# Optimization experiments

Hardware: AMD Instinct MI355X
Metric: run time of the kernel (lower is better)

## Reference

```python
import jax, jax.numpy as jnp
import numpy as np

N = 20000   # nodes
D = 512     # input_dim
H = 256     # hidden_dim = input_dim // 2
C = 7       # class_num
L = 2       # layer_num
E = 131072  # edges per class
B = 8192    # edge pairs to classify
EPS = 1e-5  # BatchNorm eps


def _bn(x, gamma, beta):
    # BatchNorm1d in training mode: batch mean / biased variance
    mu = jnp.mean(x, axis=0)
    var = jnp.mean((x - mu) ** 2, axis=0)
    return (x - mu) * jax.lax.rsqrt(var + EPS) * gamma + beta


def _gcn_conv(x, src, dst, W, b):
    # PyG GCNConv: add self-loops, symmetric deg^-1/2 normalization, aggregate at dst
    n = x.shape[0]
    loop = jnp.arange(n)
    s = jnp.concatenate([src, loop])
    d = jnp.concatenate([dst, loop])
    deg = jax.ops.segment_sum(jnp.ones(s.shape[0], x.dtype), d, num_segments=n)
    dinv = jax.lax.rsqrt(jnp.maximum(deg, 1.0))  # deg >= 1 due to self-loops
    norm = dinv[s] * dinv[d]                     # [E+N]
    xw = x @ W                                   # [N, H]
    out = jax.ops.segment_sum(norm[:, None] * xw[s], d, num_segments=n)
    return out + b


def _comp_gcn(x, edge_index, gW, gb, dW, db):
    row, col = edge_index[0], edge_index[1]
    h = jax.nn.relu(_gcn_conv(x, row, col, gW, gb))
    comp = (x[col] * x[row]) @ dW + db           # diff_proj(x[col]*x[row])
    msg = jax.ops.segment_sum(comp, row, num_segments=x.shape[0])
    return h + msg


def setup_inputs() -> dict:
    key = jax.random.key(0)
    ks = jax.random.split(key, 20)
    s = 0.05
    nrm = lambda k, shape: jax.random.normal(k, shape, jnp.float32) * s
    return {
        "x": jax.random.normal(ks[0], (N, D), jnp.float32),
        "edges": jax.random.randint(ks[1], (C, 2, E), 0, N),
        "node_id": jax.random.randint(ks[2], (2, B), 0, N),
        "lin0_W": nrm(ks[3], (C, D, H)),
        "lin0_b": nrm(ks[4], (C, H)),
        "bn_gamma": jnp.ones((C, H), jnp.float32),
        "bn_beta": jnp.zeros((C, H), jnp.float32),
        "gcn_W": nrm(ks[5], (C, L, H, H)),
        "gcn_b": nrm(ks[6], (C, L, H)),
        "dp_W": nrm(ks[7], (C, L, H, H)),
        "dp_b": nrm(ks[8], (C, L, H)),
        "fc1_W": nrm(ks[9], (C, 3 * H, 3 * H // 2)),
        "fc1_b": nrm(ks[10], (C, 3 * H // 2)),
        "fc2_W": nrm(ks[11], (C, 3 * H // 2, 3 * H // 4)),
        "fc2_b": nrm(ks[12], (C, 3 * H // 4)),
        "fc3_W": nrm(ks[13], (C, 3 * H // 4, H // 16)),
        "fc3_b": nrm(ks[14], (C, H // 16)),
        "cls_W": nrm(ks[15], ((H // 16) * C, C)),
        "cls_b": nrm(ks[16], (C,)),
    }


def reference(x, edges, node_id, lin0_W, lin0_b, bn_gamma, bn_beta,
              gcn_W, gcn_b, dp_W, dp_b, fc1_W, fc1_b, fc2_W, fc2_b,
              fc3_W, fc3_b, cls_W, cls_b):
    src, dst = node_id[0], node_id[1]
    outs = []
    for i in range(C):  # fixed small branch count
        t = jax.nn.relu(_bn(x @ lin0_W[i] + lin0_b[i], bn_gamma[i], bn_beta[i]))
        for j in range(L):
            t = _comp_gcn(t, edges[i], gcn_W[i, j], gcn_b[i, j], dp_W[i, j], dp_b[i, j])
        x1, x2 = t[src], t[dst]                        # [B, H]
        p = jnp.concatenate([x1, x2, x1 * x2], axis=1)  # [B, 3H]
        p = jax.nn.relu(p @ fc1_W[i] + fc1_b[i])
        p = jax.nn.relu(p @ fc2_W[i] + fc2_b[i])
        p = p @ fc3_W[i] + fc3_b[i]                     # [B, H//16]
        outs.append(p)
    r = jax.nn.relu(jnp.concatenate(outs, axis=1))      # [B, C*H//16]
    return r @ cls_W + cls_b                            # [B, C]
```

## Files before the change

### kernel.cpp

```cpp
#include <hip/hip_runtime.h>

typedef unsigned short u16;
typedef unsigned int   u32;
typedef __attribute__((ext_vector_type(8))) short short8;
typedef __attribute__((ext_vector_type(4))) float f32x4;

#define NNODES 20000
#define MPAD   20096
#define DIN    512
#define HID    256
#define NCLS   7
#define NLAY   2
#define NEDGE  131072
#define NPAIR  8192
#define BN_EPS 1e-5f

__device__ __forceinline__ void atomAddF(float* p, float v) { unsafeAtomicAdd(p, v); }

__device__ __forceinline__ float b2f(u16 u) {
    u32 x = ((u32)u) << 16;
    return __builtin_bit_cast(float, x);
}
__device__ __forceinline__ u16 f2b(float f) {
    u32 u = __builtin_bit_cast(u32, f);
    u32 r = u + 0x7FFFu + ((u >> 16) & 1u);
    return (u16)(r >> 16);
}
__device__ __forceinline__ float4 b2f4(ushort4 u) {
    return make_float4(b2f(u.x), b2f(u.y), b2f(u.z), b2f(u.w));
}
__device__ __forceinline__ ushort4 f2b4(float a, float b, float c, float d) {
    ushort4 o; o.x = f2b(a); o.y = f2b(b); o.z = f2b(c); o.w = f2b(d); return o;
}

__device__ __forceinline__ void async_copy16(const u16* g, u16* l) {
    __builtin_amdgcn_global_load_lds((const __attribute__((address_space(1))) void*)g,
                                     (__attribute__((address_space(3))) void*)l, 16, 0, 0);
}

__device__ __forceinline__ int chunk_swz(int orig, int nwg) {
    int xcd = orig & 7, q = nwg >> 3, r = nwg & 7;
    int base = (xcd < r) ? xcd * (q + 1) : r * (q + 1) + (xcd - r) * q;
    return base + (orig >> 3);
}

__global__ __launch_bounds__(256, 2) void gemm_fn(
    const u16* __restrict__ A, size_t sA, const u16* __restrict__ Bt, size_t sB,
    const float* __restrict__ bias, int sBias,
    float* __restrict__ Cf, u16* __restrict__ Cb, size_t sC,
    int M, int N, int K, int relu, float* statsOut)
{
    const int z = blockIdx.z;
    A  += (size_t)z * sA;
    Bt += (size_t)z * sB;
    if (bias) bias += (size_t)z * sBias;

    __shared__ u16 sm[12288];
    __shared__ float sred[512];
    u16* As = sm;
    u16* Bs = sm + 4096;

    const int tid  = threadIdx.x;
    const int wave = tid >> 6;
    const int lane = tid & 63;
    const int bm = blockIdx.x * 128;
    const int wr = (wave >> 1) * 64;
// ... 75 lines not shown
        atomAddF(&statsOut[(size_t)z * 512 + tid], sred[tid]);
        atomAddF(&statsOut[(size_t)z * 512 + 256 + tid], sred[256 + tid]);
    }

    if (Cb && N == 256) {
        u16* R = sm;
        const int lrb = (wave >> 1) * 16 + fq * 4;
        const int cb0 = wc + fr;
        #pragma unroll
        for (int mi = 0; mi < 4; ++mi) {
            __syncthreads();
            #pragma unroll
            for (int ni = 0; ni < 8; ++ni)
                #pragma unroll
                for (int rr = 0; rr < 4; ++rr) {
                    float v = acc[mi][ni][rr] + bv[ni];
                    if (relu) v = fmaxf(v, 0.f);
                    R[(lrb + rr) * 264 + cb0 + ni * 16] = f2b(v);
                }
            __syncthreads();
            #pragma unroll
            for (int p = 0; p < 4; ++p) {
                int idx = p * 256 + tid;
                int lr = idx >> 5, ch = idx & 31;
                int grow = bm + (lr >> 4) * 64 + mi * 16 + (lr & 15);
                if (grow < M)
                    *(short8*)&Cb[(size_t)z * sC + (size_t)grow * 256 + ch * 8] =
                        *(const short8*)&R[lr * 264 + ch * 8];
            }
        }
    } else {
        #pragma unroll
        for (int ni = 0; ni < 8; ++ni) {
            int col = wc + ni * 16 + fr;
            if (col >= N) continue;
            #pragma unroll
            for (int mi = 0; mi < 4; ++mi) {
                int rbase = bm + wr + mi * 16 + fq * 4;
                #pragma unroll
                for (int rr = 0; rr < 4; ++rr) {
                    int row = rbase + rr;
                    if (row >= M) continue;
                    float v = acc[mi][ni][rr] + bv[ni];
                    if (relu) v = fmaxf(v, 0.f);
                    size_t o = (size_t)z * sC + (size_t)row * N + col;
                    if (Cf) Cf[o] = v;
                    if (Cb) Cb[o] = f2b(v);
                }
            }
        }
    }
}

__global__ __launch_bounds__(256, 2) void gemm_dual(
    const u16* U, const u16* __restrict__ V, size_t sAct,
    const u16* __restrict__ Gt, const u16* __restrict__ Dt, size_t sW,
    const float* __restrict__ gbias, const float* __restrict__ dbias, int sBias,
    const float* __restrict__ degf, size_t sDeg,
    u16* Cb, int M)
{
    const int z = blockIdx.z;
    U += (size_t)z * sAct; V += (size_t)z * sAct;
    Gt += (size_t)z * sW;  Dt += (size_t)z * sW;
    gbias += (size_t)z * sBias; dbias += (size_t)z * sBias;
    degf  += (size_t)z * sDeg;
    u16* C = Cb + (size_t)z * sAct;

    __shared__ u16 sm[12288];
    u16* As = sm;
    u16* Bs = sm + 4096;

    const int tid  = threadIdx.x;
    const int wave = tid >> 6;
    const int lane = tid & 63;
    const int bm = blockIdx.x * 128;
    const int wr = (wave >> 1) * 64;
    const int wc = (wave & 1) * 128;

    const int ar = tid >> 2, aj = (tid & 3) * 8;
    u16* AsA = As + tid * 8;
    u16* AsB = As + tid * 8 + 2048;

    const int fr = lane & 15;
    const int fq = lane >> 4;
    const int kg = fq * 8;

    f32x4 zero = {0.f, 0.f, 0.f, 0.f};
    f32x4 acc[4][8];
    #pragma unroll
    for (int mi = 0; mi < 4; ++mi)
        #pragma unroll
        for (int ni = 0; ni < 8; ++ni) acc[mi][ni] = zero;

    for (int k0 = 0; k0 < HID; k0 += 32) {
        async_copy16(U + (size_t)(bm + ar) * HID + aj + k0, AsA);
        async_copy16(U + (size_t)(bm + ar + 64) * HID + aj + k0, AsB);
        #pragma unroll
        for (int c = 0; c < 4; ++c)
            async_copy16(Gt + (size_t)(c * 64 + ar) * HID + aj + k0,
                         Bs + ((size_t)c * 256 + tid) * 8);
        __syncthreads();
        short8 af[4], bfr[8];
        #pragma unroll
        for (int mi = 0; mi < 4; ++mi)
            af[mi] = *(const short8*)&As[(wr + mi * 16 + fr) * 32 + kg];
        #pragma unroll
        for (int ni = 0; ni < 8; ++ni)
            bfr[ni] = *(const short8*)&Bs[(wc + ni * 16 + fr) * 32 + kg];
        #pragma unroll
        for (int mi = 0; mi < 4; ++mi)
            #pragma unroll
            for (int ni = 0; ni < 8; ++ni)
                acc[mi][ni] = __builtin_amdgcn_mfma_f32_16x16x32_bf16(
                    af[mi], bfr[ni], acc[mi][ni], 0, 0, 0);
        __syncthreads();
    }

    {
        float gv[8];
        #pragma unroll
        for (int ni = 0; ni < 8; ++ni) gv[ni] = gbias[wc + ni * 16 + fr];
        #pragma unroll
        for (int mi = 0; mi < 4; ++mi)
            #pragma unroll
            for (int ni = 0; ni < 8; ++ni)
                #pragma unroll
                for (int rr = 0; rr < 4; ++rr)
                    acc[mi][ni][rr] = fmaxf(acc[mi][ni][rr] + gv[ni], 0.f);
    }

    for (int k0 = 0; k0 < HID; k0 += 32) {
        async_copy16(V + (size_t)(bm + ar) * HID + aj + k0, AsA);
        async_copy16(V + (size_t)(bm + ar + 64) * HID + aj + k0, AsB);
        #pragma unroll
        for (int c = 0; c < 4; ++c)
            async_copy16(Dt + (size_t)(c * 64 + ar) * HID + aj + k0,
                         Bs + ((size_t)c * 256 + tid) * 8);
        __syncthreads();
        short8 af[4], bfr[8];
        #pragma unroll
        for (int mi = 0; mi < 4; ++mi)
            af[mi] = *(const short8*)&As[(wr + mi * 16 + fr) * 32 + kg];
        #pragma unroll
        for (int ni = 0; ni < 8; ++ni)
            bfr[ni] = *(const short8*)&Bs[(wc + ni * 16 + fr) * 32 + kg];
        #pragma unroll
        for (int mi = 0; mi < 4; ++mi)
            #pragma unroll
            for (int ni = 0; ni < 8; ++ni)
                acc[mi][ni] = __builtin_amdgcn_mfma_f32_16x16x32_bf16(
                    af[mi], bfr[ni], acc[mi][ni], 0, 0, 0);
        __syncthreads();
    }

    float dv8[8];
    #pragma unroll
    for (int ni = 0; ni < 8; ++ni) dv8[ni] = dbias[wc + ni * 16 + fr];
    u16* R = sm;
    const int lrb = (wave >> 1) * 16 + fq * 4;
    const int cb0 = wc + fr;
    #pragma unroll
    for (int mi = 0; mi < 4; ++mi) {
        __syncthreads();
        float dgr[4];
        #pragma unroll
        for (int rr = 0; rr < 4; ++rr) {
            int grow = bm + wr + mi * 16 + fq * 4 + rr;
            dgr[rr] = (grow < M) ? degf[grow] : 0.f;
        }
        #pragma unroll
        for (int ni = 0; ni < 8; ++ni)
            #pragma unroll
            for (int rr = 0; rr < 4; ++rr)
                R[(lrb + rr) * 264 + cb0 + ni * 16] =
                    f2b(acc[mi][ni][rr] + dgr[rr] * dv8[ni]);
        __syncthreads();
        #pragma unroll
        for (int p = 0; p < 4; ++p) {
            int idx = p * 256 + tid;
            int lr = idx >> 5, ch = idx & 31;
            int grow = bm + (lr >> 4) * 64 + mi * 16 + (lr & 15);
            if (grow < M)
                *(short8*)&C[(size_t)grow * 256 + ch * 8] =
                    *(const short8*)&R[lr * 264 + ch * 8];
        }
    }
}

__global__ __launch_bounds__(256) void fc1_fused(
    const u16* __restrict__ tb, const int* __restrict__ src, const int* __restrict__ dst,
    const u16* __restrict__ Wt, const float* __restrict__ bias, u16* __restrict__ p1b)
{
    const int z = blockIdx.z;
    const u16* T = tb + (size_t)z * NNODES * HID;
    const u16* Bt = Wt + (size_t)z * 384 * 768;
    const float* bi = bias + (size_t)z * 384;
    u16* C = p1b + (size_t)z * NPAIR * 384;

    __shared__ u16 As[128 * 32];
    __shared__ u16 Bs[128 * 32];
    const int tid  = threadIdx.x;
    const int wave = tid >> 6;
    const int lane = tid & 63;
    const int bm = blockIdx.x * 128;
    const int bn = blockIdx.y * 128;
    const int wr = (wave >> 1) * 64;
    const int wc = (wave & 1) * 64;

    const int srow = wave * 32 + (lane >> 2);
    const int scol = (lane & 3) * 8;
    const int b0 = bm + srow, b1 = b0 + 16;
    const int s0i = src[b0], d0i = dst[b0];
    const int s1i = src[b1], d1i = dst[b1];

    const u16* Bg0 = Bt + (size_t)(bn + srow) * 768 + scol;
    const u16* Bg1 = Bg0 + (size_t)16 * 768;
    u16* As0 = &As[wave * 1024];
    u16* As1 = As0 + 512;
    u16* Bs0 = &Bs[wave * 1024];
    u16* Bs1 = Bs0 + 512;
    u16* Aw0 = As0 + lane * 8;
    u16* Aw1 = As1 + lane * 8;

    const int fr = lane & 15;
    const int kg = (lane >> 4) * 8;

    f32x4 zero = {0.f, 0.f, 0.f, 0.f};
    f32x4 acc[4][4];
    #pragma unroll
    for (int mi = 0; mi < 4; ++mi)
        #pragma unroll
        for (int ni = 0; ni < 4; ++ni) acc[mi][ni] = zero;

    for (int k0 = 0; k0 < 768; k0 += 32) {
        if (k0 < 512) {
            const u16* r0p = (k0 < 256) ? (T + (size_t)s0i * HID + k0 + scol)
                                        : (T + (size_t)d0i * HID + (k0 - 256) + scol);
            const u16* r1p = (k0 < 256) ? (T + (size_t)s1i * HID + k0 + scol)
                                        : (T + (size_t)d1i * HID + (k0 - 256) + scol);
            async_copy16(r0p, As0);
            async_copy16(r1p, As1);
        } else {
            int kk = k0 - 512 + scol;
            short8 a0 = *(const short8*)&T[(size_t)s0i * HID + kk];
            short8 c0 = *(const short8*)&T[(size_t)d0i * HID + kk];
            short8 a1 = *(const short8*)&T[(size_t)s1i * HID + kk];
            short8 c1 = *(const short8*)&T[(size_t)d1i * HID + kk];
// ... 94 lines not shown
            #pragma unroll
            for (int j = 0; j < 4; ++j) b[j] = Bs[k][tn + j];
            #pragma unroll
            for (int i = 0; i < 4; ++i)
                #pragma unroll
                for (int j = 0; j < 4; ++j)
                    acc[i][j] = fmaf(a[i], b[j], acc[i][j]);
        }
        __syncthreads();
    }
    #pragma unroll
    for (int i = 0; i < 4; ++i) {
        int gm = bm + tm + i;
        if (gm >= M) continue;
        #pragma unroll
        for (int j = 0; j < 4; ++j) {
            int gn = bn + tn + j;
            if (gn >= N) continue;
            float v = acc[i][j] + bias[gn];
            if (relu) v = fmaxf(v, 0.f);
            C[(size_t)gm * ldc + gn] = v;
        }
    }
}

__global__ void xconv(const float* __restrict__ x, u16* __restrict__ xb)
{
    int gid = blockIdx.x * blockDim.x + threadIdx.x;
    int i4 = gid * 4;
    int row = i4 >> 9;
    float4 v = make_float4(0.f, 0.f, 0.f, 0.f);
    if (row < NNODES) v = *(const float4*)&x[i4];
    *(ushort4*)&xb[i4] = f2b4(v.x, v.y, v.z, v.w);
}

__global__ void wtrans(const float* __restrict__ W, u16* __restrict__ Wt,
                       int K, int N, int NP)
{
    __shared__ float tile[32][33];
    const int m = blockIdx.z;
    const int k0 = blockIdx.x * 32, n0 = blockIdx.y * 32;
    const float* Wm = W + (size_t)m * K * N;
    u16* Wtm = Wt + (size_t)m * NP * K;
    const int c = threadIdx.x & 31, r = threadIdx.x >> 5;
    #pragma unroll
    for (int p = 0; p < 4; ++p)
        tile[r + p * 8][c] = Wm[(size_t)(k0 + r + p * 8) * N + n0 + c];
    __syncthreads();
    #pragma unroll
    for (int p = 0; p < 4; ++p)
        Wtm[(size_t)(n0 + r + p * 8) * K + k0 + c] = f2b(tile[c][r + p * 8]);
}

__device__ __forceinline__ int swz3584(int b) { return (b & 7) * 448 + (b >> 3); }

__global__ void hist(const int* __restrict__ edges, int* __restrict__ ptrs)
{
    int gid = swz3584(blockIdx.x) * 256 + threadIdx.x;
    int i = gid >> 17, e = gid & (NEDGE - 1);
    const int* eb = edges + (size_t)i * 2 * NEDGE;
    int r = eb[e], c = eb[NEDGE + e];
    atomicAdd(&ptrs[i * 20001 + c + 1], 1);
    atomicAdd(&ptrs[(7 + i) * 20001 + r + 1], 1);
}

#define SCN 512
__global__ void scan1(int* __restrict__ ptrs, int* __restrict__ aux)
{
    __shared__ int s[SCN];
    const int a = blockIdx.y;
    const int t = threadIdx.x;
    const int idx = blockIdx.x * SCN + t;
    int* arr = ptrs + a * 20001;
    int v = (idx < 20001) ? arr[idx] : 0;
    s[t] = v;
    __syncthreads();
    for (int off = 1; off < SCN; off <<= 1) {
        int x = (t >= off) ? s[t - off] : 0;
        __syncthreads();
        s[t] += x;
        __syncthreads();
    }
    if (idx < 20001) arr[idx] = s[t];
    if (t == SCN - 1) aux[a * 40 + blockIdx.x] = s[t];
}
__global__ void scan2(int* __restrict__ aux)
{
    if (threadIdx.x != 0) return;
    int a = blockIdx.x;
    int run = 0;
    for (int b = 0; b < 40; ++b) {
        int t = aux[a * 40 + b];
        aux[a * 40 + b] = run;
        run += t;
    }
}
__global__ void scan3(int* __restrict__ ptrs, const int* __restrict__ aux,
                      int* __restrict__ cur)
{
    const int a = blockIdx.y;
    const int idx = blockIdx.x * SCN + threadIdx.x;
    if (idx < 20001) {
        int v = ptrs[a * 20001 + idx] + aux[a * 40 + blockIdx.x];
        ptrs[a * 20001 + idx] = v;
        cur[a * 20001 + idx] = v;
    }
}
__global__ void csrfill(const int* __restrict__ edges, int* __restrict__ cur,
                        u16* __restrict__ othercol, u16* __restrict__ otherrow)
{
    int gid = swz3584(blockIdx.x) * 256 + threadIdx.x;
    int i = gid >> 17, e = gid & (NEDGE - 1);
    const int* eb = edges + (size_t)i * 2 * NEDGE;
    int r = eb[e], c = eb[NEDGE + e];
    int pc = atomicAdd(&cur[i * 20001 + c], 1);
    othercol[(size_t)i * NEDGE + pc] = (u16)r;
    int pr = atomicAdd(&cur[(7 + i) * 20001 + r], 1);
    otherrow[(size_t)i * NEDGE + pr] = (u16)c;
}
__global__ void mkdinv(const int* __restrict__ ptrs, float* __restrict__ dinv,
                       float* __restrict__ degf)
{
    int gid = blockIdx.x * blockDim.x + threadIdx.x;
    if (gid >= NCLS * NNODES) return;
    int i = gid / NNODES, n = gid - i * NNODES;
    int d = ptrs[i * 20001 + n + 1] - ptrs[i * 20001 + n];
    dinv[gid] = rsqrtf((float)d + 1.0f);
    int dr = ptrs[(7 + i) * 20001 + n + 1] - ptrs[(7 + i) * 20001 + n];
    degf[gid] = (float)dr;
}

__global__ void bn_relu_b(const u16* __restrict__ xwb, const float* __restrict__ stats,
                          const float* __restrict__ gamma, const float* __restrict__ beta,
                          u16* __restrict__ tb)
{
    const int z = blockIdx.y;
    const int gid = blockIdx.x * blockDim.x + threadIdx.x;
    const int n = gid >> 6, f4 = (gid & 63) * 4;
    const u16* X = xwb + (size_t)z * NNODES * HID;
    u16* T = tb + (size_t)z * NNODES * HID;
    const float* st = stats + z * 2 * HID;
    const float invN = 1.0f / NNODES;
    float4 su = *(const float4*)&st[f4];
    float4 sq = *(const float4*)&st[HID + f4];
    float4 g  = *(const float4*)&gamma[(size_t)z * HID + f4];
    float4 be = *(const float4*)&beta[(size_t)z * HID + f4];
    ushort4 u = *(const ushort4*)&X[(size_t)n * HID + f4];
    float4 x = b2f4(u);
    float o[4], mu, var;
    mu = su.x * invN; var = sq.x * invN - mu * mu;
    o[0] = fmaxf((x.x - mu) * rsqrtf(var + BN_EPS) * g.x + be.x, 0.f);
    mu = su.y * invN; var = sq.y * invN - mu * mu;
    o[1] = fmaxf((x.y - mu) * rsqrtf(var + BN_EPS) * g.y + be.y, 0.f);
    mu = su.z * invN; var = sq.z * invN - mu * mu;
    o[2] = fmaxf((x.z - mu) * rsqrtf(var + BN_EPS) * g.z + be.z, 0.f);
    mu = su.w * invN; var = sq.w * invN - mu * mu;
    o[3] = fmaxf((x.w - mu) * rsqrtf(var + BN_EPS) * g.w + be.w, 0.f);
    *(ushort4*)&T[(size_t)n * HID + f4] = f2b4(o[0], o[1], o[2], o[3]);
}

__global__ void gather2_u4(const u16* __restrict__ tb,
                           const int* __restrict__ cptrs, const u16* __restrict__ coth,
                           const int* __restrict__ rptrs, const u16* __restrict__ roth,
                           const float* __restrict__ dinv,
                           u16* __restrict__ ub, u16* __restrict__ vb, int nwg)
{
    const int logical = chunk_swz(blockIdx.x, nwg);
    const int z = logical / 5000, nb = logical % 5000;
    const size_t zo = (size_t)z * NNODES;
    const u16* T = tb + zo * HID;
    const int* cptr = cptrs + (size_t)z * 20001;
    const int* rptr = rptrs + (size_t)z * 20001;
    const u16* co = coth + (size_t)z * NEDGE;
    const u16* ro = roth + (size_t)z * NEDGE;
    const float* dv = dinv + zo;

    const int node = nb * 4 + (threadIdx.x >> 6);
    const int f = (threadIdx.x & 63) * 4;
    const float dn = dv[node];
    ushort4 tn = *(const ushort4*)&T[(size_t)node * HID + f];
    const float tnx = b2f(tn.x), tny = b2f(tn.y), tnz = b2f(tn.z), tnw = b2f(tn.w);

    float ax = dn * tnx, ay = dn * tny, az = dn * tnz, aw = dn * tnw;
    {
        const int s0 = cptr[node], s1 = cptr[node + 1];
        int e = s0;
        for (; e + 4 <= s1; e += 4) {
            int r0 = co[e], r1 = co[e + 1], r2 = co[e + 2], r3 = co[e + 3];
            float d0 = dv[r0], d1 = dv[r1], d2 = dv[r2], d3 = dv[r3];
            ushort4 u0 = *(const ushort4*)&T[(size_t)r0 * HID + f];
            ushort4 u1 = *(const ushort4*)&T[(size_t)r1 * HID + f];
            ushort4 u2 = *(const ushort4*)&T[(size_t)r2 * HID + f];
            ushort4 u3 = *(const ushort4*)&T[(size_t)r3 * HID + f];
            ax += d0 * b2f(u0.x) + d1 * b2f(u1.x) + d2 * b2f(u2.x) + d3 * b2f(u3.x);
            ay += d0 * b2f(u0.y) + d1 * b2f(u1.y) + d2 * b2f(u2.y) + d3 * b2f(u3.y);
            az += d0 * b2f(u0.z) + d1 * b2f(u1.z) + d2 * b2f(u2.z) + d3 * b2f(u3.z);
            aw += d0 * b2f(u0.w) + d1 * b2f(u1.w) + d2 * b2f(u2.w) + d3 * b2f(u3.w);
        }
        for (; e < s1; ++e) {
            int r = co[e];
            float dr = dv[r];
            ushort4 u = *(const ushort4*)&T[(size_t)r * HID + f];
            ax += dr * b2f(u.x); ay += dr * b2f(u.y);
            az += dr * b2f(u.z); aw += dr * b2f(u.w);
        }
    }
    *(ushort4*)&ub[(zo + node) * HID + f] = f2b4(dn * ax, dn * ay, dn * az, dn * aw);

    float bx = 0.f, by = 0.f, bz = 0.f, bw = 0.f;
    {
        const int s0 = rptr[node], s1 = rptr[node + 1];
        int e = s0;
        for (; e + 4 <= s1; e += 4) {
            int r0 = ro[e], r1 = ro[e + 1], r2 = ro[e + 2], r3 = ro[e + 3];
            ushort4 u0 = *(const ushort4*)&T[(size_t)r0 * HID + f];
            ushort4 u1 = *(const ushort4*)&T[(size_t)r1 * HID + f];
            ushort4 u2 = *(const ushort4*)&T[(size_t)r2 * HID + f];
            ushort4 u3 = *(const ushort4*)&T[(size_t)r3 * HID + f];
            bx += b2f(u0.x) + b2f(u1.x) + b2f(u2.x) + b2f(u3.x);
            by += b2f(u0.y) + b2f(u1.y) + b2f(u2.y) + b2f(u3.y);
            bz += b2f(u0.z) + b2f(u1.z) + b2f(u2.z) + b2f(u3.z);
            bw += b2f(u0.w) + b2f(u1.w) + b2f(u2.w) + b2f(u3.w);
        }
        for (; e < s1; ++e) {
            int cc = ro[e];
            ushort4 u = *(const ushort4*)&T[(size_t)cc * HID + f];
            bx += b2f(u.x); by += b2f(u.y);
            bz += b2f(u.z); bw += b2f(u.w);
        }
    }
    *(ushort4*)&vb[(zo + node) * HID + f] = f2b4(tnx * bx, tny * by, tnz * bz, tnw * bw);
}

__global__ void final_cls(const float* __restrict__ outs, const float* __restrict__ clsW,
                          const float* __restrict__ clsb, float* __restrict__ out)
{
    const int gid = blockIdx.x * blockDim.x + threadIdx.x;
    if (gid >= NPAIR * NCLS) return;
    const int b = gid / NCLS, c = gid % NCLS;
    float acc = clsb[c];
    const float* row = outs + (size_t)b * 112;
    #pragma unroll 4
    for (int k = 0; k < 112; ++k)
        acc = fmaf(fmaxf(row[k], 0.f), clsW[k * NCLS + c], acc);
    out[gid] = acc;
}

extern "C" void kernel_launch(void* const* d_in, const int* in_sizes, int n_in,
                              void* d_out, int out_size, void* d_ws, size_t ws_size,
                              hipStream_t stream)
{
    const float* x        = (const float*)d_in[0];
    const int*   edges    = (const int*)  d_in[1];
    const int*   node_id  = (const int*)  d_in[2];
    const float* lin0_W   = (const float*)d_in[3];
    const float* lin0_b   = (const float*)d_in[4];
    const float* bn_gamma = (const float*)d_in[5];
    const float* bn_beta  = (const float*)d_in[6];
    const float* gcn_W    = (const float*)d_in[7];
    const float* gcn_b    = (const float*)d_in[8];
    const float* dp_W     = (const float*)d_in[9];
    const float* dp_b     = (const float*)d_in[10];
    const float* fc1_W    = (const float*)d_in[11];
    const float* fc1_b    = (const float*)d_in[12];
    const float* fc2_W    = (const float*)d_in[13];
    const float* fc2_b    = (const float*)d_in[14];
    const float* fc3_W    = (const float*)d_in[15];
    const float* fc3_b    = (const float*)d_in[16];
    const float* cls_W    = (const float*)d_in[17];
    const float* cls_b    = (const float*)d_in[18];
    float* out = (float*)d_out;

    unsigned char* w = (unsigned char*)d_ws;
    size_t used = 0;
    auto alloc = [&](size_t bytes) {
        void* p = (void*)(w + used);
        used += (bytes + 255) & ~(size_t)255;
        return p;
    };
    u16*   xb       = (u16*)  alloc((size_t)MPAD * DIN * 2);
    u16*   lin0Wt   = (u16*)  alloc((size_t)NCLS * HID * DIN * 2);
    u16*   gcnWt    = (u16*)  alloc((size_t)NCLS * NLAY * HID * HID * 2);
    u16*   dpWt     = (u16*)  alloc((size_t)NCLS * NLAY * HID * HID * 2);
    u16*   fc1Wt    = (u16*)  alloc((size_t)NCLS * 384 * 768 * 2);
    u16*   fc2Wt    = (u16*)  alloc((size_t)NCLS * 256 * 384 * 2);
    int*   ptrs     = (int*)  alloc((size_t)14 * 20001 * 4);
    int*   cur      = (int*)  alloc((size_t)14 * 20001 * 4);
    int*   aux      = (int*)  alloc((size_t)14 * 40 * 4);
    u16*   othercol = (u16*)  alloc((size_t)NCLS * NEDGE * 2);
    u16*   otherrow = (u16*)  alloc((size_t)NCLS * NEDGE * 2);
    float* dinv     = (float*)alloc((size_t)NCLS * NNODES * 4);
    float* degf     = (float*)alloc((size_t)NCLS * NNODES * 4);
    float* outsb    = (float*)alloc((size_t)NPAIR * 112 * 4);
    float* stats    = (float*)alloc((size_t)NCLS * 2 * HID * 4);

    int g = 1;
    for (int t = NCLS; t >= 1; --t) {
        size_t big = ((size_t)t * NNODES + 96) * HID * 2;
        big = (big + 255) & ~(size_t)255;
        if (used + 3 * big <= ws_size) { g = t; break; }
    }
    size_t bigBytes = ((size_t)g * NNODES + 96) * HID * 2;
    u16* tbA  = (u16*)alloc(bigBytes);
    u16* ubuf = (u16*)alloc(bigBytes);
    u16* vbuf = (u16*)alloc(bigBytes);
    u16*   p1b = ubuf;
    float* p2f = (float*)vbuf;

    const int* src = node_id;
    const int* dst = node_id + NPAIR;

    xconv<<<(MPAD * DIN / 4) / 256, 256, 0, stream>>>(x, xb);
    wtrans<<<dim3(16, 8, 7),  256, 0, stream>>>(lin0_W, lin0Wt, 512, 256, 256);
    wtrans<<<dim3(8, 8, 14),  256, 0, stream>>>(gcn_W,  gcnWt,  256, 256, 256);
    wtrans<<<dim3(8, 8, 14),  256, 0, stream>>>(dp_W,   dpWt,   256, 256, 256);
    wtrans<<<dim3(24, 12, 7), 256, 0, stream>>>(fc1_W,  fc1Wt,  768, 384, 384);
    wtrans<<<dim3(12, 6, 7),  256, 0, stream>>>(fc2_W,  fc2Wt,  384, 192, 256);

    hipMemsetAsync(ptrs, 0, (size_t)14 * 20001 * 4, stream);
    hist<<<(NCLS * NEDGE) / 256, 256, 0, stream>>>(edges, ptrs);
    scan1<<<dim3(40, 14), SCN, 0, stream>>>(ptrs, aux);
    scan2<<<14, 64, 0, stream>>>(aux);
    scan3<<<dim3(40, 14), SCN, 0, stream>>>(ptrs, aux, cur);
    csrfill<<<(NCLS * NEDGE) / 256, 256, 0, stream>>>(edges, cur, othercol, otherrow);
    mkdinv<<<(NCLS * NNODES + 255) / 256, 256, 0, stream>>>(ptrs, dinv, degf);

    const size_t sT = (size_t)NNODES * HID;

    for (int cb = 0; cb < NCLS; cb += g) {
        const int gl = min(g, NCLS - cb);
        const int nwg = gl * 5000;

        hipMemsetAsync(stats, 0, (size_t)gl * 2 * HID * 4, stream);
        gemm_fn<<<dim3(157, 1, gl), 256, 0, stream>>>(
            xb, 0, lin0Wt + (size_t)cb * HID * DIN, (size_t)HID * DIN,
            lin0_b + cb * HID, HID, nullptr, ubuf, sT, NNODES, HID, DIN, 0, stats);
        bn_relu_b<<<dim3(5000, gl), 256, 0, stream>>>(
            ubuf, stats, bn_gamma + cb * HID, bn_beta + cb * HID, tbA);

        u16* t_cur = tbA;
        u16* t_alt = ubuf;
        for (int j = 0; j < NLAY; ++j) {
            const u16* gWt = gcnWt + ((size_t)cb * NLAY + j) * HID * HID;
            const u16* dWt = dpWt  + ((size_t)cb * NLAY + j) * HID * HID;
            const float* gb = gcn_b + ((size_t)cb * NLAY + j) * HID;
            const float* db = dp_b  + ((size_t)cb * NLAY + j) * HID;

            gather2_u4<<<nwg, 256, 0, stream>>>(
                t_cur, ptrs + cb * 20001, othercol + (size_t)cb * NEDGE,
                ptrs + (7 + cb) * 20001, otherrow + (size_t)cb * NEDGE,
                dinv + (size_t)cb * NNODES, t_alt, vbuf, nwg);
            gemm_dual<<<dim3(157, 1, gl), 256, 0, stream>>>(
                t_alt, vbuf, sT, gWt, dWt, (size_t)NLAY * HID * HID,
                gb, db, NLAY * HID, degf + (size_t)cb * NNODES, (size_t)NNODES,
                t_alt, NNODES);

            u16* tmp = t_cur; t_cur = t_alt; t_alt = tmp;
        }

        fc1_fused<<<dim3(64, 3, gl), 256, 0, stream>>>(
            t_cur, src, dst, fc1Wt + (size_t)cb * 384 * 768, fc1_b + cb * 384, p1b);
        gemm_fn<<<dim3(64, 1, gl), 256, 0, stream>>>(
            p1b, (size_t)NPAIR * 384, fc2Wt + (size_t)cb * 256 * 384, (size_t)256 * 384,
            fc2_b + cb * 192, 192, p2f, nullptr, (size_t)NPAIR * 192,
            NPAIR, 192, 384, 1, nullptr);
        gemm_bias_b<<<dim3(128, 1, gl), 256, 0, stream>>>(
            p2f, (size_t)NPAIR * 192, fc3_W + (size_t)cb * 192 * 16, (size_t)192 * 16,
            fc3_b + cb * 16, 16, outsb + cb * 16, 16,
            NPAIR, 16, 192, 112, 0);
    }

    final_cls<<<(NPAIR * NCLS + 255) / 256, 256, 0, stream>>>(outsb, cls_W, cls_b, out);
}
```

Measured before the change: 869.0 us.

## Pad CSR neighbor lists to multiples of four with dummy zero node

Rounds each node's adjacency list length up to a multiple of four and fills the padding with a sentinel node index that points to a zeroed padding row with zero dinv. The gather kernel can then load neighbor indices as ushort4 and drop its scalar remainder loop. Per-class node buffers are restrided to 20096 rows so the sentinel row exists in every class slab, and degrees are now taken from the fill cursors. This costs extra padding kernels, larger lists, and wasted gathers of the zero row.

```diff
diff --git a/kernel.cpp b/kernel.cpp
--- a/kernel.cpp
+++ b/kernel.cpp
@@ -2,16 +2,19 @@
 
 typedef unsigned short u16;
 typedef unsigned int   u32;
+typedef unsigned long long u64;
 typedef __attribute__((ext_vector_type(8))) short short8;
 typedef __attribute__((ext_vector_type(4))) float f32x4;
 
 #define NNODES 20000
+#define SROWS  20096
 #define MPAD   20096
 #define DIN    512
 #define HID    256
 #define NCLS   7
 #define NLAY   2
 #define NEDGE  131072
+#define LISTSZ (NEDGE + 3 * NNODES)
 #define NPAIR  8192
 #define BN_EPS 1e-5f
 
@@ -333,7 +336,7 @@
     const u16* __restrict__ Wt, const float* __restrict__ bias, u16* __restrict__ p1b)
 {
     const int z = blockIdx.z;
-    const u16* T = tb + (size_t)z * NNODES * HID;
+    const u16* T = tb + (size_t)z * SROWS * HID;
     const u16* Bt = Wt + (size_t)z * 384 * 768;
     const float* bi = bias + (size_t)z * 384;
     u16* C = p1b + (size_t)z * NPAIR * 384;
@@ -534,6 +537,19 @@
         Wtm[(size_t)(n0 + r + p * 8) * K + k0 + c] = f2b(tile[c][r + p * 8]);
 }
 
+__global__ void zeropad(u16* __restrict__ tbA, u16* __restrict__ ubuf, int g)
+{
+    const int per = 96 * (HID / 8);
+    int gid = blockIdx.x * blockDim.x + threadIdx.x;
+    if (gid >= g * per) return;
+    int z = gid / per, r = gid - z * per;
+    int row = 20000 + r / (HID / 8), col = (r % (HID / 8)) * 8;
+    size_t off = ((size_t)z * SROWS + row) * HID + col;
+    short8 zz = {0, 0, 0, 0, 0, 0, 0, 0};
+    *(short8*)&tbA[off] = zz;
+    *(short8*)&ubuf[off] = zz;
+}
+
 __device__ __forceinline__ int swz3584(int b) { return (b & 7) * 448 + (b >> 3); }
 
 __global__ void hist(const int* __restrict__ edges, int* __restrict__ ptrs)
@@ -554,7 +570,7 @@
     const int t = threadIdx.x;
     const int idx = blockIdx.x * SCN + t;
     int* arr = ptrs + a * 20001;
-    int v = (idx < 20001) ? arr[idx] : 0;
+    int v = (idx < 20001) ? ((arr[idx] + 3) & ~3) : 0;
     s[t] = v;
     __syncthreads();
     for (int off = 1; off < SCN; off <<= 1) {
@@ -596,20 +612,35 @@
     const int* eb = edges + (size_t)i * 2 * NEDGE;
     int r = eb[e], c = eb[NEDGE + e];
     int pc = atomicAdd(&cur[i * 20001 + c], 1);
-    othercol[(size_t)i * NEDGE + pc] = (u16)r;
+    othercol[(size_t)i * LISTSZ + pc] = (u16)r;
     int pr = atomicAdd(&cur[(7 + i) * 20001 + r], 1);
-    otherrow[(size_t)i * NEDGE + pr] = (u16)c;
-}
-__global__ void mkdinv(const int* __restrict__ ptrs, float* __restrict__ dinv,
-                       float* __restrict__ degf)
+    otherrow[(size_t)i * LISTSZ + pr] = (u16)c;
+}
+__global__ void padfill(const int* __restrict__ ptrs, const int* __restrict__ cur,
+                        u16* __restrict__ othercol, u16* __restrict__ otherrow)
 {
     int gid = blockIdx.x * blockDim.x + threadIdx.x;
-    if (gid >= NCLS * NNODES) return;
-    int i = gid / NNODES, n = gid - i * NNODES;
-    int d = ptrs[i * 20001 + n + 1] - ptrs[i * 20001 + n];
-    dinv[gid] = rsqrtf((float)d + 1.0f);
-    int dr = ptrs[(7 + i) * 20001 + n + 1] - ptrs[(7 + i) * 20001 + n];
-    degf[gid] = (float)dr;
+    if (gid >= 14 * NNODES) return;
+    int a = gid / NNODES, n = gid - a * NNODES;
+    int p = cur[a * 20001 + n], e = ptrs[a * 20001 + n + 1];
+    u16* lst = (a < 7) ? (othercol + (size_t)a * LISTSZ)
+                       : (otherrow + (size_t)(a - 7) * LISTSZ);
+    for (; p < e; ++p) lst[p] = (u16)NNODES;
+}
+__global__ void mkdinv(const int* __restrict__ ptrs, const int* __restrict__ cur,
+                       float* __restrict__ dinv, float* __restrict__ degf)
+{
+    int gid = blockIdx.x * blockDim.x + threadIdx.x;
+    if (gid >= NCLS * SROWS) return;
+    int i = gid / SROWS, n = gid - i * SROWS;
+    if (n < NNODES) {
+        int d = cur[i * 20001 + n] - ptrs[i * 20001 + n];
+        dinv[gid] = rsqrtf((float)d + 1.0f);
+        int dr = cur[(7 + i) * 20001 + n] - ptrs[(7 + i) * 20001 + n];
+        degf[(size_t)i * NNODES + n] = (float)dr;
+    } else {
+        dinv[gid] = 0.f;
+    }
 }
 
 __global__ void bn_relu_b(const u16* __restrict__ xwb, const float* __restrict__ stats,
@@ -619,8 +650,8 @@
     const int z = blockIdx.y;
     const int gid = blockIdx.x * blockDim.x + threadIdx.x;
     const int n = gid >> 6, f4 = (gid & 63) * 4;
-    const u16* X = xwb + (size_t)z * NNODES * HID;
-    u16* T = tb + (size_t)z * NNODES * HID;
+    const u16* X = xwb + (size_t)z * SROWS * HID;
+    u16* T = tb + (size_t)z * SROWS * HID;
     const float* st = stats + z * 2 * HID;
     const float invN = 1.0f / NNODES;
     float4 su = *(const float4*)&st[f4];
@@ -649,12 +680,12 @@
 {
     const int logical = chunk_swz(blockIdx.x, nwg);
     const int z = logical / 5000, nb = logical % 5000;
-    const size_t zo = (size_t)z * NNODES;
+    const size_t zo = (size_t)z * SROWS;
     const u16* T = tb + zo * HID;
     const int* cptr = cptrs + (size_t)z * 20001;
     const int* rptr = rptrs + (size_t)z * 20001;
-    const u16* co = coth + (size_t)z * NEDGE;
-    const u16* ro = roth + (size_t)z * NEDGE;
+    const u16* co = coth + (size_t)z * LISTSZ;
+    const u16* ro = roth + (size_t)z * LISTSZ;
     const float* dv = dinv + zo;
 
     const int node = nb * 4 + (threadIdx.x >> 6);
@@ -666,9 +697,9 @@
     float ax = dn * tnx, ay = dn * tny, az = dn * tnz, aw = dn * tnw;
     {
         const int s0 = cptr[node], s1 = cptr[node + 1];
-        int e = s0;
-        for (; e + 4 <= s1; e += 4) {
-            int r0 = co[e], r1 = co[e + 1], r2 = co[e + 2], r3 = co[e + 3];
+        for (int e = s0; e < s1; e += 4) {
+            ushort4 i4 = *(const ushort4*)&co[e];
+            int r0 = i4.x, r1 = i4.y, r2 = i4.z, r3 = i4.w;
             float d0 = dv[r0], d1 = dv[r1], d2 = dv[r2], d3 = dv[r3];
             ushort4 u0 = *(const ushort4*)&T[(size_t)r0 * HID + f];
             ushort4 u1 = *(const ushort4*)&T[(size_t)r1 * HID + f];
@@ -679,22 +710,15 @@
             az += d0 * b2f(u0.z) + d1 * b2f(u1.z) + d2 * b2f(u2.z) + d3 * b2f(u3.z);
             aw += d0 * b2f(u0.w) + d1 * b2f(u1.w) + d2 * b2f(u2.w) + d3 * b2f(u3.w);
         }
-        for (; e < s1; ++e) {
-            int r = co[e];
-            float dr = dv[r];
-            ushort4 u = *(const ushort4*)&T[(size_t)r * HID + f];
-            ax += dr * b2f(u.x); ay += dr * b2f(u.y);
-            az += dr * b2f(u.z); aw += dr * b2f(u.w);
-        }
     }
     *(ushort4*)&ub[(zo + node) * HID + f] = f2b4(dn * ax, dn * ay, dn * az, dn * aw);
 
     float bx = 0.f, by = 0.f, bz = 0.f, bw = 0.f;
     {
         const int s0 = rptr[node], s1 = rptr[node + 1];
-        int e = s0;
-        for (; e + 4 <= s1; e += 4) {
-            int r0 = ro[e], r1 = ro[e + 1], r2 = ro[e + 2], r3 = ro[e + 3];
+        for (int e = s0; e < s1; e += 4) {
+            ushort4 i4 = *(const ushort4*)&ro[e];
+            int r0 = i4.x, r1 = i4.y, r2 = i4.z, r3 = i4.w;
             ushort4 u0 = *(const ushort4*)&T[(size_t)r0 * HID + f];
             ushort4 u1 = *(const ushort4*)&T[(size_t)r1 * HID + f];
             ushort4 u2 = *(const ushort4*)&T[(size_t)r2 * HID + f];
@@ -703,12 +727,6 @@
             by += b2f(u0.y) + b2f(u1.y) + b2f(u2.y) + b2f(u3.y);
             bz += b2f(u0.z) + b2f(u1.z) + b2f(u2.z) + b2f(u3.z);
             bw += b2f(u0.w) + b2f(u1.w) + b2f(u2.w) + b2f(u3.w);
-        }
-        for (; e < s1; ++e) {
-            int cc = ro[e];
-            ushort4 u = *(const ushort4*)&T[(size_t)cc * HID + f];
-            bx += b2f(u.x); by += b2f(u.y);
-            bz += b2f(u.z); bw += b2f(u.w);
         }
     }
     *(ushort4*)&vb[(zo + node) * HID + f] = f2b4(tnx * bx, tny * by, tnz * bz, tnw * bw);
@@ -769,20 +787,20 @@
     int*   ptrs     = (int*)  alloc((size_t)14 * 20001 * 4);
     int*   cur      = (int*)  alloc((size_t)14 * 20001 * 4);
     int*   aux      = (int*)  alloc((size_t)14 * 40 * 4);
-    u16*   othercol = (u16*)  alloc((size_t)NCLS * NEDGE * 2);
-    u16*   otherrow = (u16*)  alloc((size_t)NCLS * NEDGE * 2);
-    float* dinv     = (float*)alloc((size_t)NCLS * NNODES * 4);
+    u16*   othercol = (u16*)  alloc((size_t)NCLS * LISTSZ * 2);
+    u16*   otherrow = (u16*)  alloc((size_t)NCLS * LISTSZ * 2);
+    float* dinv     = (float*)alloc((size_t)NCLS * SROWS * 4);
     float* degf     = (float*)alloc((size_t)NCLS * NNODES * 4);
     float* outsb    = (float*)alloc((size_t)NPAIR * 112 * 4);
     float* stats    = (float*)alloc((size_t)NCLS * 2 * HID * 4);
 
     int g = 1;
     for (int t = NCLS; t >= 1; --t) {
-        size_t big = ((size_t)t * NNODES + 96) * HID * 2;
+        size_t big = (size_t)t * SROWS * HID * 2;
         big = (big + 255) & ~(size_t)255;
         if (used + 3 * big <= ws_size) { g = t; break; }
     }
-    size_t bigBytes = ((size_t)g * NNODES + 96) * HID * 2;
+    size_t bigBytes = (size_t)g * SROWS * HID * 2;
     u16* tbA  = (u16*)alloc(bigBytes);
     u16* ubuf = (u16*)alloc(bigBytes);
     u16* vbuf = (u16*)alloc(bigBytes);
@@ -798,6 +816,7 @@
     wtrans<<<dim3(8, 8, 14),  256, 0, stream>>>(dp_W,   dpWt,   256, 256, 256);
     wtrans<<<dim3(24, 12, 7), 256, 0, stream>>>(fc1_W,  fc1Wt,  768, 384, 384);
     wtrans<<<dim3(12, 6, 7),  256, 0, stream>>>(fc2_W,  fc2Wt,  384, 192, 256);
+    zeropad<<<(g * 3072 + 255) / 256, 256, 0, stream>>>(tbA, ubuf, g);
 
     hipMemsetAsync(ptrs, 0, (size_t)14 * 20001 * 4, stream);
     hist<<<(NCLS * NEDGE) / 256, 256, 0, stream>>>(edges, ptrs);
@@ -805,9 +824,10 @@
     scan2<<<14, 64, 0, stream>>>(aux);
     scan3<<<dim3(40, 14), SCN, 0, stream>>>(ptrs, aux, cur);
     csrfill<<<(NCLS * NEDGE) / 256, 256, 0, stream>>>(edges, cur, othercol, otherrow);
-    mkdinv<<<(NCLS * NNODES + 255) / 256, 256, 0, stream>>>(ptrs, dinv, degf);
-
-    const size_t sT = (size_t)NNODES * HID;
+    padfill<<<(14 * NNODES + 255) / 256, 256, 0, stream>>>(ptrs, cur, othercol, otherrow);
+    mkdinv<<<(NCLS * SROWS + 255) / 256, 256, 0, stream>>>(ptrs, cur, dinv, degf);
+
+    const size_t sT = (size_t)SROWS * HID;
 
     for (int cb = 0; cb < NCLS; cb += g) {
         const int gl = min(g, NCLS - cb);
@@ -829,9 +849,9 @@
             const float* db = dp_b  + ((size_t)cb * NLAY + j) * HID;
 
             gather2_u4<<<nwg, 256, 0, stream>>>(
-                t_cur, ptrs + cb * 20001, othercol + (size_t)cb * NEDGE,
-                ptrs + (7 + cb) * 20001, otherrow + (size_t)cb * NEDGE,
-                dinv + (size_t)cb * NNODES, t_alt, vbuf, nwg);
+                t_cur, ptrs + cb * 20001, othercol + (size_t)cb * LISTSZ,
+                ptrs + (7 + cb) * 20001, otherrow + (size_t)cb * LISTSZ,
+                dinv + (size_t)cb * SROWS, t_alt, vbuf, nwg);
             gemm_dual<<<dim3(157, 1, gl), 256, 0, stream>>>(
                 t_alt, vbuf, sT, gWt, dWt, (size_t)NLAY * HID * HID,
                 gb, db, NLAY * HID, degf + (size_t)cb * NNODES, (size_t)NNODES,
```

After: 887.0 us. +2.1%, slower.

## Fuse sparse neighbor gather into dual GCN GEMM kernel via shared memory

Applied to the files above, without the earlier changes.

Merges the separate gather kernel and the dual GEMM kernel into one. Each block aggregates 64 nodes' normalized neighbor features directly into LDS, runs the GCN GEMM, then re-gathers the composition message into LDS for the diff-projection GEMM. This removes the round trip of the intermediate U/V activation buffers through global memory and one kernel launch per layer. In exchange the GEMM tile shrinks from 128 to 64 rows, LDS use per block grows, and the gather phases run serially with MFMA work inside each block, which can hurt latency hiding.

```diff
diff --git a/kernel.cpp b/kernel.cpp
--- a/kernel.cpp
+++ b/kernel.cpp
@@ -2,6 +2,7 @@
 
 typedef unsigned short u16;
 typedef unsigned int   u32;
+typedef unsigned long long u64;
 typedef __attribute__((ext_vector_type(8))) short short8;
 typedef __attribute__((ext_vector_type(4))) float f32x4;
 
@@ -193,63 +194,107 @@
     }
 }
 
-__global__ __launch_bounds__(256, 2) void gemm_dual(
-    const u16* U, const u16* __restrict__ V, size_t sAct,
+__global__ __launch_bounds__(256, 3) void gather_dual(
+    const u16* __restrict__ T, size_t sAct,
+    const int* __restrict__ cptrs, const u16* __restrict__ coth,
+    const int* __restrict__ rptrs, const u16* __restrict__ roth,
+    const float* __restrict__ dinv,
     const u16* __restrict__ Gt, const u16* __restrict__ Dt, size_t sW,
     const float* __restrict__ gbias, const float* __restrict__ dbias, int sBias,
-    const float* __restrict__ degf, size_t sDeg,
-    u16* Cb, int M)
-{
-    const int z = blockIdx.z;
-    U += (size_t)z * sAct; V += (size_t)z * sAct;
-    Gt += (size_t)z * sW;  Dt += (size_t)z * sW;
-    gbias += (size_t)z * sBias; dbias += (size_t)z * sBias;
-    degf  += (size_t)z * sDeg;
-    u16* C = Cb + (size_t)z * sAct;
-
-    __shared__ u16 sm[12288];
-    u16* As = sm;
-    u16* Bs = sm + 4096;
+    const float* __restrict__ degf,
+    u16* __restrict__ C, int nwg)
+{
+    const int logical = chunk_swz(blockIdx.x, nwg);
+    const int z = logical / 313, bx = logical % 313;
+    const int bm = bx * 64;
+
+    const u16* Tz = T + (size_t)z * sAct;
+    const int* cptr = cptrs + (size_t)z * 20001;
+    const int* rptr = rptrs + (size_t)z * 20001;
+    const u16* co = coth + (size_t)z * NEDGE;
+    const u16* ro = roth + (size_t)z * NEDGE;
+    const float* dv = dinv + (size_t)z * NNODES;
+    const u16* G = Gt + (size_t)z * sW;
+    const u16* D = Dt + (size_t)z * sW;
+    const float* gb = gbias + (size_t)z * sBias;
+    const float* db = dbias + (size_t)z * sBias;
+    const float* dgf = degf + (size_t)z * NNODES;
+    u16* Cz = C + (size_t)z * sAct;
+
+    __shared__ u16 sm[25088];
+    u16* Au = sm;
+    u16* Bs = sm + 16896;
 
     const int tid  = threadIdx.x;
     const int wave = tid >> 6;
     const int lane = tid & 63;
-    const int bm = blockIdx.x * 128;
-    const int wr = (wave >> 1) * 64;
-    const int wc = (wave & 1) * 128;
+    const int f = lane * 4;
 
     const int ar = tid >> 2, aj = (tid & 3) * 8;
-    u16* AsA = As + tid * 8;
-    u16* AsB = As + tid * 8 + 2048;
-
     const int fr = lane & 15;
     const int fq = lane >> 4;
     const int kg = fq * 8;
+    const int wr = (wave >> 1) * 32;
+    const int wc = (wave & 1) * 128;
+
+    for (int i = 0; i < 16; ++i) {
+        const int nl = wave * 16 + i;
+        const int node = bm + nl;
+        float ax = 0.f, ay = 0.f, az = 0.f, aw = 0.f;
+        if (node < NNODES) {
+            const float dn = dv[node];
+            ushort4 tn = *(const ushort4*)&Tz[(size_t)node * HID + f];
+            ax = dn * b2f(tn.x); ay = dn * b2f(tn.y);
+            az = dn * b2f(tn.z); aw = dn * b2f(tn.w);
+            const int s0 = cptr[node], s1 = cptr[node + 1];
+            int e = s0;
+            for (; e + 4 <= s1; e += 4) {
+                int r0 = co[e], r1 = co[e + 1], r2 = co[e + 2], r3 = co[e + 3];
+                float d0 = dv[r0], d1 = dv[r1], d2 = dv[r2], d3 = dv[r3];
+                ushort4 u0 = *(const ushort4*)&Tz[(size_t)r0 * HID + f];
+                ushort4 u1 = *(const ushort4*)&Tz[(size_t)r1 * HID + f];
+                ushort4 u2 = *(const ushort4*)&Tz[(size_t)r2 * HID + f];
+                ushort4 u3 = *(const ushort4*)&Tz[(size_t)r3 * HID + f];
+                ax += d0 * b2f(u0.x) + d1 * b2f(u1.x) + d2 * b2f(u2.x) + d3 * b2f(u3.x);
+                ay += d0 * b2f(u0.y) + d1 * b2f(u1.y) + d2 * b2f(u2.y) + d3 * b2f(u3.y);
+                az += d0 * b2f(u0.z) + d1 * b2f(u1.z) + d2 * b2f(u2.z) + d3 * b2f(u3.z);
+                aw += d0 * b2f(u0.w) + d1 * b2f(u1.w) + d2 * b2f(u2.w) + d3 * b2f(u3.w);
+            }
+            for (; e < s1; ++e) {
+                int r = co[e];
+                float dr = dv[r];
+                ushort4 u = *(const ushort4*)&Tz[(size_t)r * HID + f];
+                ax += dr * b2f(u.x); ay += dr * b2f(u.y);
+                az += dr * b2f(u.z); aw += dr * b2f(u.w);
+            }
+            ax *= dn; ay *= dn; az *= dn; aw *= dn;
+        }
+        *(ushort4*)&Au[nl * 264 + f] = f2b4(ax, ay, az, aw);
+    }
+    __syncthreads();
 
     f32x4 zero = {0.f, 0.f, 0.f, 0.f};
-    f32x4 acc[4][8];
-    #pragma unroll
-    for (int mi = 0; mi < 4; ++mi)
+    f32x4 acc[2][8];
+    #pragma unroll
+    for (int mi = 0; mi < 2; ++mi)
         #pragma unroll
         for (int ni = 0; ni < 8; ++ni) acc[mi][ni] = zero;
 
     for (int k0 = 0; k0 < HID; k0 += 32) {
-        async_copy16(U + (size_t)(bm + ar) * HID + aj + k0, AsA);
-        async_copy16(U + (size_t)(bm + ar + 64) * HID + aj + k0, AsB);
         #pragma unroll
         for (int c = 0; c < 4; ++c)
-            async_copy16(Gt + (size_t)(c * 64 + ar) * HID + aj + k0,
+            async_copy16(G + (size_t)(c * 64 + ar) * HID + aj + k0,
                          Bs + ((size_t)c * 256 + tid) * 8);
         __syncthreads();
-        short8 af[4], bfr[8];
-        #pragma unroll
-        for (int mi = 0; mi < 4; ++mi)
-            af[mi] = *(const short8*)&As[(wr + mi * 16 + fr) * 32 + kg];
+        short8 af[2], bfr[8];
+        #pragma unroll
+        for (int mi = 0; mi < 2; ++mi)
+            af[mi] = *(const short8*)&Au[(wr + mi * 16 + fr) * 264 + k0 + kg];
         #pragma unroll
         for (int ni = 0; ni < 8; ++ni)
             bfr[ni] = *(const short8*)&Bs[(wc + ni * 16 + fr) * 32 + kg];
         #pragma unroll
-        for (int mi = 0; mi < 4; ++mi)
+        for (int mi = 0; mi < 2; ++mi)
             #pragma unroll
             for (int ni = 0; ni < 8; ++ni)
                 acc[mi][ni] = __builtin_amdgcn_mfma_f32_16x16x32_bf16(
@@ -260,9 +305,9 @@
     {
         float gv[8];
         #pragma unroll
-        for (int ni = 0; ni < 8; ++ni) gv[ni] = gbias[wc + ni * 16 + fr];
-        #pragma unroll
-        for (int mi = 0; mi < 4; ++mi)
+        for (int ni = 0; ni < 8; ++ni) gv[ni] = gb[wc + ni * 16 + fr];
+        #pragma unroll
+        for (int mi = 0; mi < 2; ++mi)
             #pragma unroll
             for (int ni = 0; ni < 8; ++ni)
                 #pragma unroll
@@ -270,23 +315,53 @@
                     acc[mi][ni][rr] = fmaxf(acc[mi][ni][rr] + gv[ni], 0.f);
     }
 
+    for (int i = 0; i < 16; ++i) {
+        const int nl = wave * 16 + i;
+        const int node = bm + nl;
+        float bxx = 0.f, byy = 0.f, bzz = 0.f, bww = 0.f;
+        if (node < NNODES) {
+            ushort4 tn = *(const ushort4*)&Tz[(size_t)node * HID + f];
+            const int s0 = rptr[node], s1 = rptr[node + 1];
+            int e = s0;
+            for (; e + 4 <= s1; e += 4) {
+                int r0 = ro[e], r1 = ro[e + 1], r2 = ro[e + 2], r3 = ro[e + 3];
+                ushort4 u0 = *(const ushort4*)&Tz[(size_t)r0 * HID + f];
+                ushort4 u1 = *(const ushort4*)&Tz[(size_t)r1 * HID + f];
+                ushort4 u2 = *(const ushort4*)&Tz[(size_t)r2 * HID + f];
+                ushort4 u3 = *(const ushort4*)&Tz[(size_t)r3 * HID + f];
+                bxx += b2f(u0.x) + b2f(u1.x) + b2f(u2.x) + b2f(u3.x);
+                byy += b2f(u0.y) + b2f(u1.y) + b2f(u2.y) + b2f(u3.y);
+                bzz += b2f(u0.z) + b2f(u1.z) + b2f(u2.z) + b2f(u3.z);
+                bww += b2f(u0.w) + b2f(u1.w) + b2f(u2.w) + b2f(u3.w);
+            }
+            for (; e < s1; ++e) {
+                int cc = ro[e];
+                ushort4 u = *(const ushort4*)&Tz[(size_t)cc * HID + f];
+                bxx += b2f(u.x); byy += b2f(u.y);
+                bzz += b2f(u.z); bww += b2f(u.w);
+            }
+            bxx *= b2f(tn.x); byy *= b2f(tn.y);
+            bzz *= b2f(tn.z); bww *= b2f(tn.w);
+        }
+        *(ushort4*)&Au[nl * 264 + f] = f2b4(bxx, byy, bzz, bww);
+    }
+    __syncthreads();
+
     for (int k0 = 0; k0 < HID; k0 += 32) {
-        async_copy16(V + (size_t)(bm + ar) * HID + aj + k0, AsA);
-        async_copy16(V + (size_t)(bm + ar + 64) * HID + aj + k0, AsB);
         #pragma unroll
         for (int c = 0; c < 4; ++c)
-            async_copy16(Dt + (size_t)(c * 64 + ar) * HID + aj + k0,
+            async_copy16(D + (size_t)(c * 64 + ar) * HID + aj + k0,
                          Bs + ((size_t)c * 256 + tid) * 8);
         __syncthreads();
-        short8 af[4], bfr[8];
-        #pragma unroll
-        for (int mi = 0; mi < 4; ++mi)
-            af[mi] = *(const short8*)&As[(wr + mi * 16 + fr) * 32 + kg];
+        short8 af[2], bfr[8];
+        #pragma unroll
+        for (int mi = 0; mi < 2; ++mi)
+            af[mi] = *(const short8*)&Au[(wr + mi * 16 + fr) * 264 + k0 + kg];
         #pragma unroll
         for (int ni = 0; ni < 8; ++ni)
             bfr[ni] = *(const short8*)&Bs[(wc + ni * 16 + fr) * 32 + kg];
         #pragma unroll
-        for (int mi = 0; mi < 4; ++mi)
+        for (int mi = 0; mi < 2; ++mi)
             #pragma unroll
             for (int ni = 0; ni < 8; ++ni)
                 acc[mi][ni] = __builtin_amdgcn_mfma_f32_16x16x32_bf16(
@@ -296,35 +371,30 @@
 
     float dv8[8];
     #pragma unroll
-    for (int ni = 0; ni < 8; ++ni) dv8[ni] = dbias[wc + ni * 16 + fr];
+    for (int ni = 0; ni < 8; ++ni) dv8[ni] = db[wc + ni * 16 + fr];
     u16* R = sm;
-    const int lrb = (wave >> 1) * 16 + fq * 4;
-    const int cb0 = wc + fr;
-    #pragma unroll
-    for (int mi = 0; mi < 4; ++mi) {
-        __syncthreads();
-        float dgr[4];
+    #pragma unroll
+    for (int mi = 0; mi < 2; ++mi) {
         #pragma unroll
         for (int rr = 0; rr < 4; ++rr) {
-            int grow = bm + wr + mi * 16 + fq * 4 + rr;
-            dgr[rr] = (grow < M) ? degf[grow] : 0.f;
-        }
-        #pragma unroll
-        for (int ni = 0; ni < 8; ++ni)
-            #pragma unroll
-            for (int rr = 0; rr < 4; ++rr)
-                R[(lrb + rr) * 264 + cb0 + ni * 16] =
-                    f2b(acc[mi][ni][rr] + dgr[rr] * dv8[ni]);
-        __syncthreads();
-        #pragma unroll
-        for (int p = 0; p < 4; ++p) {
-            int idx = p * 256 + tid;
-            int lr = idx >> 5, ch = idx & 31;
-            int grow = bm + (lr >> 4) * 64 + mi * 16 + (lr & 15);
-            if (grow < M)
-                *(short8*)&C[(size_t)grow * 256 + ch * 8] =
-                    *(const short8*)&R[lr * 264 + ch * 8];
-        }
+            int rl = wr + mi * 16 + fq * 4 + rr;
+            int grow = bm + rl;
+            float dg = (grow < NNODES) ? dgf[grow] : 0.f;
+            #pragma unroll
+            for (int ni = 0; ni < 8; ++ni)
+                R[rl * 264 + wc + ni * 16 + fr] =
+                    f2b(acc[mi][ni][rr] + dg * dv8[ni]);
+        }
+    }
+    __syncthreads();
+    #pragma unroll
+    for (int p = 0; p < 8; ++p) {
+        int idx = p * 256 + tid;
+        int lr = idx >> 5, ch = idx & 31;
+        int grow = bm + lr;
+        if (grow < NNODES)
+            *(short8*)&Cz[(size_t)grow * 256 + ch * 8] =
+                *(const short8*)&R[lr * 264 + ch * 8];
     }
 }
 
@@ -641,79 +711,6 @@
     *(ushort4*)&T[(size_t)n * HID + f4] = f2b4(o[0], o[1], o[2], o[3]);
 }
 
-__global__ void gather2_u4(const u16* __restrict__ tb,
-                           const int* __restrict__ cptrs, const u16* __restrict__ coth,
-                           const int* __restrict__ rptrs, const u16* __restrict__ roth,
-                           const float* __restrict__ dinv,
-                           u16* __restrict__ ub, u16* __restrict__ vb, int nwg)
-{
-    const int logical = chunk_swz(blockIdx.x, nwg);
-    const int z = logical / 5000, nb = logical % 5000;
-    const size_t zo = (size_t)z * NNODES;
-    const u16* T = tb + zo * HID;
-    const int* cptr = cptrs + (size_t)z * 20001;
-    const int* rptr = rptrs + (size_t)z * 20001;
-    const u16* co = coth + (size_t)z * NEDGE;
-    const u16* ro = roth + (size_t)z * NEDGE;
-    const float* dv = dinv + zo;
-
-    const int node = nb * 4 + (threadIdx.x >> 6);
-    const int f = (threadIdx.x & 63) * 4;
-    const float dn = dv[node];
-    ushort4 tn = *(const ushort4*)&T[(size_t)node * HID + f];
-    const float tnx = b2f(tn.x), tny = b2f(tn.y), tnz = b2f(tn.z), tnw = b2f(tn.w);
-
-    float ax = dn * tnx, ay = dn * tny, az = dn * tnz, aw = dn * tnw;
-    {
-        const int s0 = cptr[node], s1 = cptr[node + 1];
-        int e = s0;
-        for (; e + 4 <= s1; e += 4) {
-            int r0 = co[e], r1 = co[e + 1], r2 = co[e + 2], r3 = co[e + 3];
-            float d0 = dv[r0], d1 = dv[r1], d2 = dv[r2], d3 = dv[r3];
-            ushort4 u0 = *(const ushort4*)&T[(size_t)r0 * HID + f];
-            ushort4 u1 = *(const ushort4*)&T[(size_t)r1 * HID + f];
-            ushort4 u2 = *(const ushort4*)&T[(size_t)r2 * HID + f];
-            ushort4 u3 = *(const ushort4*)&T[(size_t)r3 * HID + f];
-            ax += d0 * b2f(u0.x) + d1 * b2f(u1.x) + d2 * b2f(u2.x) + d3 * b2f(u3.x);
-            ay += d0 * b2f(u0.y) + d1 * b2f(u1.y) + d2 * b2f(u2.y) + d3 * b2f(u3.y);
-            az += d0 * b2f(u0.z) + d1 * b2f(u1.z) + d2 * b2f(u2.z) + d3 * b2f(u3.z);
-            aw += d0 * b2f(u0.w) + d1 * b2f(u1.w) + d2 * b2f(u2.w) + d3 * b2f(u3.w);
-        }
-        for (; e < s1; ++e) {
-            int r = co[e];
-            float dr = dv[r];
-            ushort4 u = *(const ushort4*)&T[(size_t)r * HID + f];
-            ax += dr * b2f(u.x); ay += dr * b2f(u.y);
-            az += dr * b2f(u.z); aw += dr * b2f(u.w);
-        }
-    }
-    *(ushort4*)&ub[(zo + node) * HID + f] = f2b4(dn * ax, dn * ay, dn * az, dn * aw);
-
-    float bx = 0.f, by = 0.f, bz = 0.f, bw = 0.f;
-    {
-        const int s0 = rptr[node], s1 = rptr[node + 1];
-        int e = s0;
-        for (; e + 4 <= s1; e += 4) {
-            int r0 = ro[e], r1 = ro[e + 1], r2 = ro[e + 2], r3 = ro[e + 3];
-            ushort4 u0 = *(const ushort4*)&T[(size_t)r0 * HID + f];
-            ushort4 u1 = *(const ushort4*)&T[(size_t)r1 * HID + f];
-            ushort4 u2 = *(const ushort4*)&T[(size_t)r2 * HID + f];
-            ushort4 u3 = *(const ushort4*)&T[(size_t)r3 * HID + f];
-            bx += b2f(u0.x) + b2f(u1.x) + b2f(u2.x) + b2f(u3.x);
-            by += b2f(u0.y) + b2f(u1.y) + b2f(u2.y) + b2f(u3.y);
-            bz += b2f(u0.z) + b2f(u1.z) + b2f(u2.z) + b2f(u3.z);
-            bw += b2f(u0.w) + b2f(u1.w) + b2f(u2.w) + b2f(u3.w);
-        }
-        for (; e < s1; ++e) {
-            int cc = ro[e];
-            ushort4 u = *(const ushort4*)&T[(size_t)cc * HID + f];
-            bx += b2f(u.x); by += b2f(u.y);
-            bz += b2f(u.z); bw += b2f(u.w);
-        }
-    }
-    *(ushort4*)&vb[(zo + node) * HID + f] = f2b4(tnx * bx, tny * by, tnz * bz, tnw * bw);
-}
-
 __global__ void final_cls(const float* __restrict__ outs, const float* __restrict__ clsW,
                           const float* __restrict__ clsb, float* __restrict__ out)
 {
@@ -786,8 +783,8 @@
     u16* tbA  = (u16*)alloc(bigBytes);
     u16* ubuf = (u16*)alloc(bigBytes);
     u16* vbuf = (u16*)alloc(bigBytes);
-    u16*   p1b = ubuf;
-    float* p2f = (float*)vbuf;
+    u16*   p1b = vbuf;
+    float* p2f = (float*)ubuf;
 
     const int* src = node_id;
     const int* dst = node_id + NPAIR;
@@ -811,7 +808,7 @@
 
     for (int cb = 0; cb < NCLS; cb += g) {
         const int gl = min(g, NCLS - cb);
-        const int nwg = gl * 5000;
+        const int nwg = gl * 313;
 
         hipMemsetAsync(stats, 0, (size_t)gl * 2 * HID * 4, stream);
         gemm_fn<<<dim3(157, 1, gl), 256, 0, stream>>>(
@@ -823,20 +820,18 @@
         u16* t_cur = tbA;
         u16* t_alt = ubuf;
         for (int j = 0; j < NLAY; ++j) {
-            const u16* gWt = gcnWt + ((size_t)cb * NLAY + j) * HID * HID;
-            const u16* dWt = dpWt  + ((size_t)cb * NLAY + j) * HID * HID;
-            const float* gb = gcn_b + ((size_t)cb * NLAY + j) * HID;
-            const float* db = dp_b  + ((size_t)cb * NLAY + j) * HID;
-
-            gather2_u4<<<nwg, 256, 0, stream>>>(
-                t_cur, ptrs + cb * 20001, othercol + (size_t)cb * NEDGE,
+            gather_dual<<<nwg, 256, 0, stream>>>(
+                t_cur, sT,
+                ptrs + cb * 20001, othercol + (size_t)cb * NEDGE,
                 ptrs + (7 + cb) * 20001, otherrow + (size_t)cb * NEDGE,
-                dinv + (size_t)cb * NNODES, t_alt, vbuf, nwg);
-            gemm_dual<<<dim3(157, 1, gl), 256, 0, stream>>>(
-                t_alt, vbuf, sT, gWt, dWt, (size_t)NLAY * HID * HID,
-                gb, db, NLAY * HID, degf + (size_t)cb * NNODES, (size_t)NNODES,
-                t_alt, NNODES);
-
+                dinv + (size_t)cb * NNODES,
+                gcnWt + ((size_t)cb * NLAY + j) * HID * HID,
+                dpWt  + ((size_t)cb * NLAY + j) * HID * HID,
+                (size_t)NLAY * HID * HID,
+                gcn_b + ((size_t)cb * NLAY + j) * HID,
+                dp_b  + ((size_t)cb * NLAY + j) * HID, NLAY * HID,
+                degf + (size_t)cb * NNODES,
+                t_alt, nwg);
             u16* tmp = t_cur; t_cur = t_alt; t_alt = tmp;
         }
 
```

New measurement: 1.034 ms. 1.19x slower.
